# Kernel tuning notes

Hardware: AMD Instinct MI355X
Metric: run time of the kernel (lower is better)

Reference implementation:

```python
import jax, jax.numpy as jnp
import numpy as np

B, S, IN_F, OUT_F = 4, 2048, 4096, 4096

def setup_inputs() -> dict:
    key = jax.random.key(0)
    k1, k2, k3 = jax.random.split(key, 3)
    # int8 activations and weights (symmetric range)
    x = jax.random.randint(k1, (B, S, IN_F), -128, 128, dtype=jnp.int32).astype(jnp.int8)
    weight_q = jax.random.randint(k2, (OUT_F, IN_F), -128, 128, dtype=jnp.int32).astype(jnp.int8)
    scale_x = jnp.float32(0.05)   # activation quant scale
    scale_w = jnp.float32(0.02)   # weight quant scale (scalar, per-tensor)
    scale_y = jax.random.uniform(k3, (OUT_F,), minval=0.5, maxval=2.0, dtype=jnp.float32)  # per-output-row scale
    return {"x": x, "weight_q": weight_q, "scale_x": scale_x, "scale_w": scale_w, "scale_y": scale_y}

def reference(x, weight_q, scale_x, scale_w, scale_y):
    # int8 GEMM with int32 accumulation: [B,S,IN] @ [OUT,IN]^T -> [B,S,OUT]
    acc = jax.lax.dot_general(x, weight_q, ((((2,), (1,)), ((), ()))),
                              preferred_element_type=jnp.int32)
    # fused requantization scale: scale_x * scale_w / scale_y  -> [OUT]
    requant_scale = (scale_x * scale_w / scale_y).astype(jnp.float32)
    out_f = acc.astype(jnp.float32) * requant_scale  # broadcast over last dim
    out_q = jnp.clip(jnp.round(out_f), -128, 127).astype(jnp.int8)
    return out_q, scale_y
```

## Files before the change

kernel.cpp:

```cpp
#include <hip/hip_runtime.h>
#include <cstdint>


#define MDIM 8192
#define NDIM 4096
#define KDIM 4096
#define BM 256
#define BN 256
#define NH 64

typedef int v4i __attribute__((ext_vector_type(4)));

__device__ __forceinline__ uint32_t pack4(int a, int b, int c, int d) {
  return (uint32_t)(a & 0xFF) | ((uint32_t)(b & 0xFF) << 8) |
         ((uint32_t)(c & 0xFF) << 16) | ((uint32_t)(d & 0xFF) << 24);
}

__global__ __launch_bounds__(256) void pack_kernel(
    const int* __restrict__ x32, const int* __restrict__ w32,
    const float* __restrict__ sy, uint8_t* __restrict__ x8f,
    uint8_t* __restrict__ w8f, float* __restrict__ tail) {
  const int t = blockIdx.x * 256 + threadIdx.x;
  if (t < NDIM) tail[t] = sy[t];
  const int NXC = (MDIM / 16) * KDIM;
  const int NWC = (NDIM / 16) * KDIM;
  if (t >= NXC + NWC) return;
  const int* src;
  uint8_t* dst;
  int chunk;
  if (t < NXC) {
    chunk = t;
    src = x32;
    dst = x8f;
  } else {
    chunk = t - NXC;
    src = w32;
    dst = w8f;
  }
  const int lpos = chunk & 63;
  const int rf = (chunk >> 6) & 15;
  const int h = (chunk >> 10) & 63;
  const int mb = chunk >> 16;
  const int kl = lpos >> 4, fr = lpos & 15;
  const int r = mb * 256 + rf * 16 + fr;
  const int k0 = h * 64 + kl * 16;
  const int* s = src + (size_t)r * KDIM + k0;
  v4i a0 = *(const v4i*)(s + 0);
  v4i a1 = *(const v4i*)(s + 4);
  v4i a2 = *(const v4i*)(s + 8);
  v4i a3 = *(const v4i*)(s + 12);
  v4i o;
  o[0] = (int)pack4(a0[0], a0[1], a0[2], a0[3]);
  o[1] = (int)pack4(a1[0], a1[1], a1[2], a1[3]);
  o[2] = (int)pack4(a2[0], a2[1], a2[2], a2[3]);
  o[3] = (int)pack4(a3[0], a3[1], a3[2], a3[3]);
  *(v4i*)(dst + (size_t)chunk * 16) = o;
}

__global__ __launch_bounds__(256, 1) void gemm_kernel(
    const uint8_t* __restrict__ A8, const uint8_t* __restrict__ B8,
    const float* __restrict__ sxp, const float* __restrict__ swp,
    const float* __restrict__ syp, float* __restrict__ out) {
  const int tid = threadIdx.x;
  const int lane = tid & 63;
  const int wave = tid >> 6;

  const int wg = ((int)blockIdx.x % 8) * 64 + (int)blockIdx.x / 8;
  const int mb = wg >> 4;
  const int nb = wg & 15;

  const int wm2 = wave >> 1;
  const int wn2 = wave & 1;

  const uint8_t* Asrc =
      A8 + ((size_t)mb << 20) + ((size_t)wm2 << 13) + (size_t)lane * 16;
  const uint8_t* Bsrc =
      B8 + ((size_t)nb << 20) + ((size_t)wn2 << 13) + (size_t)lane * 16;

  v4i acc[8][8];
#pragma unroll
  for (int i = 0; i < 8; i++)
#pragma unroll
    for (int j = 0; j < 8; j++) acc[i][j] = (v4i){0, 0, 0, 0};

  v4i a0[8], b0[8], a1[8], b1[8];

  auto load = [&](v4i(&a)[8], v4i(&b)[8], int h) {
    const uint8_t* pa = Asrc + ((size_t)h << 14);
    const uint8_t* pb = Bsrc + ((size_t)h << 14);
#pragma unroll
    for (int i = 0; i < 8; i++) a[i] = *(const v4i*)(pa + (i << 10));
#pragma unroll
    for (int j = 0; j < 8; j++) b[j] = *(const v4i*)(pb + (j << 10));
  };
  auto mfma = [&](v4i(&a)[8], v4i(&b)[8]) {
#pragma unroll
    for (int i = 0; i < 8; i++)
#pragma unroll
      for (int j = 0; j < 8; j++)
        acc[i][j] =
            __builtin_amdgcn_mfma_i32_16x16x64_i8(a[i], b[j], acc[i][j], 0, 0, 0);
  };

  load(a0, b0, 0);
  load(a1, b1, 1);

  for (int h = 0; h < NH - 2; h += 2) {
    mfma(a0, b0);
    load(a0, b0, h + 2);
    mfma(a1, b1);
    load(a1, b1, h + 3);
  }
  mfma(a0, b0);
  mfma(a1, b1);

  const float s = sxp[0] * swp[0];
  const int kl = lane >> 4;
  const int fr = lane & 15;
  const int wrow = mb * 256 + wm2 * 128;
  const int wcol = nb * 256 + wn2 * 128;
#pragma unroll
  for (int j = 0; j < 8; j++) {
    const int col = wcol + j * 16 + fr;
    const float rs = s / syp[col];
#pragma unroll
    for (int i = 0; i < 8; i++) {
      const int row0 = wrow + i * 16 + kl * 4;
#pragma unroll
      for (int r = 0; r < 4; r++) {
        float v = rintf((float)acc[i][j][r] * rs);
        v = fminf(127.f, fmaxf(-128.f, v));
        out[(size_t)(row0 + r) * NDIM + col] = v;
      }
    }
  }
}

extern "C" void kernel_launch(void* const* d_in, const int* in_sizes, int n_in,
                              void* d_out, int out_size, void* d_ws, size_t ws_size,
                              hipStream_t stream) {
  const int* x32 = (const int*)d_in[0];
  const int* w32 = (const int*)d_in[1];
  const float* sx = (const float*)d_in[2];
  const float* sw = (const float*)d_in[3];
  const float* sy = (const float*)d_in[4];
  float* out = (float*)d_out;
  float* tail = out + (size_t)MDIM * NDIM;

  uint8_t* x8f = (uint8_t*)d_ws;
  uint8_t* w8f = x8f + (size_t)MDIM * KDIM;

  const int total = (MDIM / 16) * KDIM + (NDIM / 16) * KDIM;
  pack_kernel<<<total / 256, 256, 0, stream>>>(x32, w32, sy, x8f, w8f, tail);

  const int nblocks = (MDIM / BM) * (NDIM / BN);
  gemm_kernel<<<nblocks, 256, 0, stream>>>(x8f, w8f, sx, sw, sy, out);
}
```

Before: 185.8 us.

## Stage GEMM tiles through LDS with async global_load_lds and 8 waves

In the old kernel each of four waves loaded its A and B fragments straight from global memory into registers, so a workgroup fetched the same data several times. Now a 512-thread workgroup cooperatively copies each K-slice of the A and B tiles into double-buffered LDS with global_load_lds. The eight waves then read their fragments from LDS, which is meant to cut redundant global traffic and raise the number of waves per CU. In exchange it adds barriers and explicit waitcnt management, and it relies on hand-tuned vmcnt counts being correct for the async copies.

```diff
diff --git a/kernel.cpp b/kernel.cpp
--- a/kernel.cpp
+++ b/kernel.cpp
@@ -10,6 +10,17 @@
 #define NH 64
 
 typedef int v4i __attribute__((ext_vector_type(4)));
+
+#define FENCE() asm volatile("" ::: "memory")
+#define BARX()                    \
+  do {                            \
+    FENCE();                      \
+    __builtin_amdgcn_s_barrier(); \
+    FENCE();                      \
+  } while (0)
+#define LGKM0() asm volatile("s_waitcnt lgkmcnt(0)" ::: "memory")
+#define VMCNT4() asm volatile("s_waitcnt vmcnt(4)" ::: "memory")
+#define VMCNT0() asm volatile("s_waitcnt vmcnt(0)" ::: "memory")
 
 __device__ __forceinline__ uint32_t pack4(int a, int b, int c, int d) {
   return (uint32_t)(a & 0xFF) | ((uint32_t)(b & 0xFF) << 8) |
@@ -57,10 +68,12 @@
   *(v4i*)(dst + (size_t)chunk * 16) = o;
 }
 
-__global__ __launch_bounds__(256, 1) void gemm_kernel(
+__global__ __launch_bounds__(512, 2) void gemm_kernel(
     const uint8_t* __restrict__ A8, const uint8_t* __restrict__ B8,
     const float* __restrict__ sxp, const float* __restrict__ swp,
     const float* __restrict__ syp, float* __restrict__ out) {
+  __shared__ __align__(16) uint8_t lds[65536];
+
   const int tid = threadIdx.x;
   const int lane = tid & 63;
   const int wave = tid >> 6;
@@ -69,58 +82,95 @@
   const int mb = wg >> 4;
   const int nb = wg & 15;
 
-  const int wm2 = wave >> 1;
-  const int wn2 = wave & 1;
-
-  const uint8_t* Asrc =
-      A8 + ((size_t)mb << 20) + ((size_t)wm2 << 13) + (size_t)lane * 16;
-  const uint8_t* Bsrc =
-      B8 + ((size_t)nb << 20) + ((size_t)wn2 << 13) + (size_t)lane * 16;
-
-  v4i acc[8][8];
+  const int wm2 = wave >> 2;
+  const int wn4 = wave & 3;
+
+  const uint8_t* Abase = A8 + ((size_t)mb << 20);
+  const uint8_t* Bbase = B8 + ((size_t)nb << 20);
+
+  const uint32_t tid16 = (uint32_t)tid * 16;
+  const uint32_t lane16 = (uint32_t)lane * 16;
+  const uint32_t aoff = ((uint32_t)(wm2 * 8) << 10) + lane16;
+  const uint32_t boff = 16384u + ((uint32_t)(wn4 * 4) << 10) + lane16;
+
+  v4i acc[8][4];
 #pragma unroll
   for (int i = 0; i < 8; i++)
 #pragma unroll
-    for (int j = 0; j < 8; j++) acc[i][j] = (v4i){0, 0, 0, 0};
-
-  v4i a0[8], b0[8], a1[8], b1[8];
-
-  auto load = [&](v4i(&a)[8], v4i(&b)[8], int h) {
-    const uint8_t* pa = Asrc + ((size_t)h << 14);
-    const uint8_t* pb = Bsrc + ((size_t)h << 14);
-#pragma unroll
-    for (int i = 0; i < 8; i++) a[i] = *(const v4i*)(pa + (i << 10));
-#pragma unroll
-    for (int j = 0; j < 8; j++) b[j] = *(const v4i*)(pb + (j << 10));
+    for (int j = 0; j < 4; j++) acc[i][j] = (v4i){0, 0, 0, 0};
+
+  auto gload = [&](const uint8_t* src, uint32_t ldsoff) {
+    __builtin_amdgcn_global_load_lds(
+        (const __attribute__((address_space(1))) void*)src,
+        (__attribute__((address_space(3))) void*)(lds + ldsoff), 16, 0, 0);
   };
-  auto mfma = [&](v4i(&a)[8], v4i(&b)[8]) {
-#pragma unroll
-    for (int i = 0; i < 8; i++)
-#pragma unroll
-      for (int j = 0; j < 8; j++)
-        acc[i][j] =
-            __builtin_amdgcn_mfma_i32_16x16x64_i8(a[i], b[j], acc[i][j], 0, 0, 0);
+  auto stage = [&](int h) {
+    const uint32_t lb = (uint32_t)(h & 1) * 32768u;
+    const uint8_t* sa = Abase + ((size_t)h << 14) + tid16;
+    const uint8_t* sb = Bbase + ((size_t)h << 14) + tid16;
+    gload(sa, lb + tid16);
+    gload(sa + 8192, lb + 8192u + tid16);
+    gload(sb, lb + 16384u + tid16);
+    gload(sb + 8192, lb + 24576u + tid16);
   };
 
-  load(a0, b0, 0);
-  load(a1, b1, 1);
-
-  for (int h = 0; h < NH - 2; h += 2) {
-    mfma(a0, b0);
-    load(a0, b0, h + 2);
-    mfma(a1, b1);
-    load(a1, b1, h + 3);
+  v4i af0[8], bf0[4], af1[8], bf1[4];
+
+#define READ_FRAGS(AF, BF, SB)                                   \
+  do {                                                           \
+    _Pragma("unroll") for (int i = 0; i < 8; i++) AF[i] =        \
+        *(const v4i*)(lds + (SB) + aoff + (i << 10));            \
+    _Pragma("unroll") for (int j = 0; j < 4; j++) BF[j] =        \
+        *(const v4i*)(lds + (SB) + boff + (j << 10));            \
+  } while (0)
+
+#define MFMA32(AF, BF)                                                        \
+  do {                                                                        \
+    _Pragma("unroll") for (int i = 0; i < 8; i++) _Pragma(                    \
+        "unroll") for (int j = 0; j < 4; j++) acc[i][j] =                     \
+        __builtin_amdgcn_mfma_i32_16x16x64_i8(AF[i], BF[j], acc[i][j], 0, 0, \
+                                              0);                             \
+  } while (0)
+
+  stage(0);
+  stage(1);
+  VMCNT4();
+  BARX();
+  READ_FRAGS(af0, bf0, 0u);
+
+  for (int h = 0; h < 62; h += 2) {
+    LGKM0();
+    BARX();
+    stage(h + 2);
+    VMCNT4();
+    BARX();
+    READ_FRAGS(af1, bf1, 32768u);
+    MFMA32(af0, bf0);
+
+    LGKM0();
+    BARX();
+    stage(h + 3);
+    VMCNT4();
+    BARX();
+    READ_FRAGS(af0, bf0, 0u);
+    MFMA32(af1, bf1);
   }
-  mfma(a0, b0);
-  mfma(a1, b1);
+
+  LGKM0();
+  BARX();
+  VMCNT0();
+  BARX();
+  READ_FRAGS(af1, bf1, 32768u);
+  MFMA32(af0, bf0);
+  MFMA32(af1, bf1);
 
   const float s = sxp[0] * swp[0];
   const int kl = lane >> 4;
   const int fr = lane & 15;
   const int wrow = mb * 256 + wm2 * 128;
-  const int wcol = nb * 256 + wn2 * 128;
-#pragma unroll
-  for (int j = 0; j < 8; j++) {
+  const int wcol = nb * 256 + wn4 * 64;
+#pragma unroll
+  for (int j = 0; j < 4; j++) {
     const int col = wcol + j * 16 + fr;
     const float rs = s / syp[col];
 #pragma unroll
@@ -154,5 +204,5 @@
   pack_kernel<<<total / 256, 256, 0, stream>>>(x32, w32, sy, x8f, w8f, tail);
 
   const int nblocks = (MDIM / BM) * (NDIM / BN);
-  gemm_kernel<<<nblocks, 256, 0, stream>>>(x8f, w8f, sx, sw, sy, out);
-}
+  gemm_kernel<<<nblocks, 512, 0, stream>>>(x8f, w8f, sx, sw, sy, out);
+}
```

New measurement: 184.2 us. No clear change (-0.8%).
